# Optimization experiments

Measured on AMD Instinct MI355X. Metric: run time of the kernel, lower is better.

## Reference

```python
import jax, jax.numpy as jnp
import numpy as np

B, T, D, H = 4, 2048, 1024, 16
DH = D // H


def setup_inputs() -> dict:
    key = jax.random.key(0)
    ks = jax.random.split(key, 11)
    s = 1.0 / np.sqrt(D)
    return {
        "q": jax.random.normal(ks[0], (B, T, D), jnp.float32),
        "k": jax.random.normal(ks[1], (B, T, D), jnp.float32),
        "v": jax.random.normal(ks[2], (B, T, D), jnp.float32),
        "Wq": jax.random.normal(ks[3], (D, D), jnp.float32) * s,
        "bq": jax.random.normal(ks[4], (D,), jnp.float32) * s,
        "Wk": jax.random.normal(ks[5], (D, D), jnp.float32) * s,
        "bk": jax.random.normal(ks[6], (D,), jnp.float32) * s,
        "Wv": jax.random.normal(ks[7], (D, D), jnp.float32) * s,
        "bv": jax.random.normal(ks[8], (D,), jnp.float32) * s,
        "Wo": jax.random.normal(ks[9], (D, D), jnp.float32) * s,
        "bo": jax.random.normal(ks[10], (D,), jnp.float32) * s,
    }


def _heads(x):
    # (B, T, D) -> (B, H, T, DH)
    return x.reshape(B, T, H, DH).transpose(0, 2, 1, 3)


def reference(q, k, v, Wq, bq, Wk, bk, Wv, bv, Wo, bo):
    qh = _heads(q @ Wq + bq)
    kh = _heads(k @ Wk + bk)
    vh = _heads(v @ Wv + bv)
    scale = 1.0 / np.sqrt(DH).astype(np.float32)
    # full (B, H, T, T) score matrix, as in the original module
    scores = jnp.einsum("bhqd,bhkd->bhqk", qh, kh) * scale
    causal = jnp.tril(jnp.ones((T, T), dtype=bool))  # keep j <= i (causal intent)
    scores = jnp.where(causal, scores, -jnp.inf)
    attn = jax.nn.softmax(scores, axis=-1)
    ctx = jnp.einsum("bhqk,bhkd->bhqd", attn, vh)
    ctx = ctx.transpose(0, 2, 1, 3).reshape(B, T, D)
    return ctx @ Wo + bo
```

## Files before the change

### kernel.cpp

```cpp
#include <hip/hip_runtime.h>
#include <hip/hip_bf16.h>

#define NB 4
#define NT 2048
#define ND 1024
#define NH 16
#define NDH 64
#define NM (NB*NT)

typedef __bf16 bf16_t;
typedef bf16_t bf16x4 __attribute__((ext_vector_type(4)));
typedef bf16_t bf16x8 __attribute__((ext_vector_type(8)));
typedef float f32x2 __attribute__((ext_vector_type(2)));
typedef float f32x4 __attribute__((ext_vector_type(4)));
typedef unsigned int u32x4 __attribute__((ext_vector_type(4)));

__device__ __forceinline__ void gload_lds16(const bf16_t* g, bf16_t* l) {
  __builtin_amdgcn_global_load_lds(
      (const __attribute__((address_space(1))) unsigned int*)g,
      (__attribute__((address_space(3))) unsigned int*)l, 16, 0, 0);
}

__device__ __forceinline__ f32x2 lo2(f32x4 v) { return __builtin_shufflevector(v, v, 0, 1); }
__device__ __forceinline__ f32x2 hi2(f32x4 v) { return __builtin_shufflevector(v, v, 2, 3); }

__device__ __forceinline__ float exp2_hw(float x) {
  float r;
  asm("v_exp_f32 %0, %1" : "=v"(r) : "v"(x));
  return r;
}

__global__ void transpose_cvt4(const float* __restrict__ w0, const float* __restrict__ w1,
                               const float* __restrict__ w2, const float* __restrict__ w3,
                               bf16_t* __restrict__ o0, bf16_t* __restrict__ o1,
                               bf16_t* __restrict__ o2, bf16_t* __restrict__ o3) {
  __shared__ float tile[32][33];
  const float* in = blockIdx.z == 0 ? w0 : blockIdx.z == 1 ? w1 : blockIdx.z == 2 ? w2 : w3;
  bf16_t* out     = blockIdx.z == 0 ? o0 : blockIdx.z == 1 ? o1 : blockIdx.z == 2 ? o2 : o3;
  int n0 = blockIdx.x * 32, k0 = blockIdx.y * 32;
  int tx = threadIdx.x & 31, ty = threadIdx.x >> 5;
  #pragma unroll
  for (int r = ty; r < 32; r += 8)
    tile[r][tx] = in[(size_t)(k0 + r) * ND + n0 + tx];
  __syncthreads();
  #pragma unroll
  for (int r = ty; r < 32; r += 8)
    out[(size_t)(n0 + r) * ND + k0 + tx] = (bf16_t)tile[tx][r];
}

#define ALD 36
__global__ __launch_bounds__(256) void gemm_qkv(
    const float* __restrict__ Aq, const float* __restrict__ Ak, const float* __restrict__ Av,
    const bf16_t* __restrict__ Bq, const bf16_t* __restrict__ Bk, const bf16_t* __restrict__ Bv,
    const float* __restrict__ bq, const float* __restrict__ bk, const float* __restrict__ bv,
    bf16_t* __restrict__ Qh, bf16_t* __restrict__ Kh, bf16_t* __restrict__ Vt,
    float qscale) {
  __shared__ bf16_t As[128 * ALD];
  __shared__ bf16_t Bs[128 * 32];
  const int z = blockIdx.z;
  const float*  A    = z == 0 ? Aq : z == 1 ? Ak : Av;
  const bf16_t* Bt   = z == 0 ? Bq : z == 1 ? Bk : Bv;
  const float*  bias = z == 0 ? bq : z == 1 ? bk : bv;
  const float   scale = z == 0 ? qscale : 1.0f;
  bf16_t* outp = z == 0 ? Qh : z == 1 ? Kh : Vt;

  const int tid  = threadIdx.x;
  const int lane = tid & 63;
  const int wid  = tid >> 6;
  const int tm = blockIdx.x * 128;
  const int tn = blockIdx.y * 128;
  const int wr = wid >> 1, wc = wid & 1;
  const int lrow = lane & 15;
  const int lko  = (lane >> 4) << 3;

  const int cB  = wid * 64 + lane;
  const int rB0 = cB >> 2;
  const int kB0 = (cB & 3) << 3;

  const int arow = tid >> 1;
  const int acb  = (tid & 1) << 4;
  const float* abase = A + (size_t)(tm + arow) * ND + acb;

  f32x4 acc[4][4];
  #pragma unroll
  for (int i = 0; i < 4; ++i)
    #pragma unroll
    for (int j = 0; j < 4; ++j) {
      f32x4 z4 = {0.f, 0.f, 0.f, 0.f};
      acc[i][j] = z4;
    }

  float4 ar0 = ((const float4*)abase)[0];
  float4 ar1 = ((const float4*)abase)[1];
  float4 ar2 = ((const float4*)abase)[2];
  float4 ar3 = ((const float4*)abase)[3];

  for (int k0 = 0; k0 < ND; k0 += 32) {
    gload_lds16(Bt + (size_t)(tn + rB0)      * ND + k0 + kB0, Bs + wid * 512);
    gload_lds16(Bt + (size_t)(tn + rB0 + 64) * ND + k0 + kB0, Bs + 2048 + wid * 512);

    bf16x8 w0, w1;
    w0[0] = (bf16_t)ar0.x; w0[1] = (bf16_t)ar0.y; w0[2] = (bf16_t)ar0.z; w0[3] = (bf16_t)ar0.w;
    w0[4] = (bf16_t)ar1.x; w0[5] = (bf16_t)ar1.y; w0[6] = (bf16_t)ar1.z; w0[7] = (bf16_t)ar1.w;
    w1[0] = (bf16_t)ar2.x; w1[1] = (bf16_t)ar2.y; w1[2] = (bf16_t)ar2.z; w1[3] = (bf16_t)ar2.w;
    w1[4] = (bf16_t)ar3.x; w1[5] = (bf16_t)ar3.y; w1[6] = (bf16_t)ar3.z; w1[7] = (bf16_t)ar3.w;
    *(bf16x8*)&As[arow * ALD + acb]     = w0;
    *(bf16x8*)&As[arow * ALD + acb + 8] = w1;

    asm volatile("s_waitcnt vmcnt(0) lgkmcnt(0)\n\ts_barrier" ::: "memory");

    if (k0 + 32 < ND) {
      const float4* ap = (const float4*)(abase + k0 + 32);
      ar0 = ap[0]; ar1 = ap[1]; ar2 = ap[2]; ar3 = ap[3];
    }

    bf16x8 af[4], bfr[4];
    #pragma unroll
    for (int i = 0; i < 4; ++i)
      af[i] = *(const bf16x8*)&As[(wr * 64 + i * 16 + lrow) * ALD + lko];
    #pragma unroll
    for (int j = 0; j < 4; ++j)
      bfr[j] = *(const bf16x8*)&Bs[(wc * 64 + j * 16 + lrow) * 32 + lko];
    #pragma unroll
    for (int i = 0; i < 4; ++i)
      #pragma unroll
      for (int j = 0; j < 4; ++j)
        acc[i][j] = __builtin_amdgcn_mfma_f32_16x16x32_bf16(af[i], bfr[j], acc[i][j], 0, 0, 0);

    asm volatile("s_waitcnt lgkmcnt(0)\n\ts_barrier" ::: "memory");
  }

  const int rb = (lane >> 4) << 2;
  #pragma unroll
  for (int j = 0; j < 4; ++j) {
    int n = tn + wc * 64 + j * 16 + lrow;
    float bv = bias[n];
    int h = n >> 6, dh = n & (NDH - 1);
    #pragma unroll
    for (int i = 0; i < 4; ++i) {
      int m0 = tm + wr * 64 + i * 16 + rb;
      int b = m0 >> 11, t0 = m0 & (NT - 1);
      if (z == 2) {
        bf16x4 o;
        #pragma unroll
        for (int r = 0; r < 4; ++r) o[r] = (bf16_t)((acc[i][j][r] + bv) * scale);
        size_t idx = ((size_t)(b * NH + h) * NDH + dh) * NT + t0;
        *(bf16x4*)(outp + idx) = o;
      } else {
        #pragma unroll
        for (int r = 0; r < 4; ++r) {
          float val = (acc[i][j][r] + bv) * scale;
          size_t idx = ((size_t)(b * NH + h) * NT + t0 + r) * NDH + dh;
          outp[idx] = (bf16_t)val;
        }
      }
    }
  }
}

__global__ __launch_bounds__(256) void gemm_out(const bf16_t* __restrict__ A,
                                                const bf16_t* __restrict__ Bt,
                                                const float* __restrict__ bias,
                                                float* __restrict__ outp) {
  __shared__ bf16_t As[128 * 32];
  __shared__ bf16_t Bs[128 * 32];
  const int tid  = threadIdx.x;
  const int lane = tid & 63;
  const int wid  = tid >> 6;
  const int tm = blockIdx.x * 128;
  const int tn = blockIdx.y * 128;
  const int wr = wid >> 1, wc = wid & 1;
  const int lrow = lane & 15;
  const int lko  = (lane >> 4) << 3;

  const int cA  = wid * 64 + lane;
  const int rA0 = cA >> 2;
  const int kA0 = (cA & 3) << 3;

  f32x4 acc[4][4];
  #pragma unroll
  for (int i = 0; i < 4; ++i)
    #pragma unroll
    for (int j = 0; j < 4; ++j) {
      f32x4 z = {0.f, 0.f, 0.f, 0.f};
      acc[i][j] = z;
    }

  for (int k0 = 0; k0 < ND; k0 += 32) {
    gload_lds16(A  + (size_t)(tm + rA0)      * ND + k0 + kA0, As + wid * 512);
    gload_lds16(A  + (size_t)(tm + rA0 + 64) * ND + k0 + kA0, As + 2048 + wid * 512);
    gload_lds16(Bt + (size_t)(tn + rA0)      * ND + k0 + kA0, Bs + wid * 512);
    gload_lds16(Bt + (size_t)(tn + rA0 + 64) * ND + k0 + kA0, Bs + 2048 + wid * 512);
    __syncthreads();
    bf16x8 af[4], bfr[4];
    #pragma unroll
    for (int i = 0; i < 4; ++i)
      af[i] = *(const bf16x8*)&As[(wr * 64 + i * 16 + lrow) * 32 + lko];
    #pragma unroll
    for (int j = 0; j < 4; ++j)
      bfr[j] = *(const bf16x8*)&Bs[(wc * 64 + j * 16 + lrow) * 32 + lko];
    #pragma unroll
    for (int i = 0; i < 4; ++i)
      #pragma unroll
      for (int j = 0; j < 4; ++j)
        acc[i][j] = __builtin_amdgcn_mfma_f32_16x16x32_bf16(af[i], bfr[j], acc[i][j], 0, 0, 0);
    __syncthreads();
  }

  const int rb = (lane >> 4) << 2;
  #pragma unroll
  for (int j = 0; j < 4; ++j) {
    int n = tn + wc * 64 + j * 16 + lrow;
    float bv = bias[n];
    #pragma unroll
    for (int i = 0; i < 4; ++i) {
      #pragma unroll
      for (int r = 0; r < 4; ++r) {
        int m = tm + wr * 64 + i * 16 + rb + r;
        outp[(size_t)m * ND + n] = acc[i][j][r] + bv;
      }
    }
  }
}


__device__ __forceinline__ bf16x8 lds_swz_read(const bf16_t* base, int row, int colb) {
  return *(const bf16x8*)((const char*)base + row * 128 + (colb ^ ((row & 7) << 4)));
}

#define CVTPK(lo, hi) ({ unsigned r_; \
  asm("v_cvt_pk_bf16_f32 %0, %1, %2" : "=v"(r_) : "v"(lo), "v"(hi)); r_; })

__global__ __launch_bounds__(256) void attn_kernel(
    const bf16_t* __restrict__ Qh, const bf16_t* __restrict__ Kh,
    const bf16_t* __restrict__ Vt, bf16_t* __restrict__ ctx) {
  __shared__ bf16_t Ks[2][64 * 64];
  __shared__ bf16_t Vs[2][64 * 64];
  const int tid  = threadIdx.x;
  const int lane = tid & 63;
  const int wid  = tid >> 6;

  const int work    = (blockIdx.x & 7) * 128 + (blockIdx.x >> 3);
  const int bh      = work >> 4;
  const int pairIdx = work & 15;
  const int b = bh >> 4, h = bh & 15;

  const bf16_t* Qbh = Qh + (size_t)bh * NT * NDH;
  const bf16_t* Kbh = Kh + (size_t)bh * NT * NDH;
  const bf16_t* Vbh = Vt + (size_t)bh * NDH * NT;

  const int lrow = lane & 15;
  const int lg   = lane >> 4;

  const char *kS0, *kS1, *vS0, *vS1;
  {
    int o0 = wid * 1024 + lane * 16;
    int o1 = 4096 + wid * 1024 + lane * 16;
    int r0_ = o0 >> 7, r1_ = o1 >> 7;
    kS0 = (const char*)Kbh + (o0 ^ ((r0_ & 7) << 4));
    kS1 = (const char*)Kbh + (o1 ^ ((r1_ & 7) << 4));
    int c0 = (o0 & 127) ^ ((r0_ & 7) << 4);
    int c1 = (o1 & 127) ^ ((r1_ & 7) << 4);
    vS0 = (const char*)Vbh + (size_t)r0_ * (NT * 2) + c0;
    vS1 = (const char*)Vbh + (size_t)r1_ * (NT * 2) + c1;
  }
  const int ldsOff = wid * 512;

  auto stage = [&](int t, int buf) {
    bf16_t* kb = Ks[buf];
    bf16_t* vb = Vs[buf];
    size_t kOff = (size_t)t * 8192;
    size_t vOff = (size_t)t * 128;
    gload_lds16((const bf16_t*)(kS0 + kOff), kb + ldsOff);
    gload_lds16((const bf16_t*)(kS1 + kOff), kb + 2048 + ldsOff);
    gload_lds16((const bf16_t*)(vS0 + vOff), vb + ldsOff);
    gload_lds16((const bf16_t*)(vS1 + vOff), vb + 2048 + ldsOff);
  };

  #pragma unroll 1
  for (int half = 0; half < 2; ++half) {
    const int qidx = half ? (31 - pairIdx) : pairIdx;
    const int r0   = qidx * 64 + wid * 16;
    const int qg   = r0 + lrow;

    bf16x8 qf0 = *(const bf16x8*)&Qbh[(size_t)(r0 + lrow) * NDH + lg * 8];
    bf16x8 qf1 = *(const bf16x8*)&Qbh[(size_t)(r0 + lrow) * NDH + 32 + lg * 8];

    float lsum = 0.f;
    f32x4 acc[4];
    #pragma unroll
    for (int d = 0; d < 4; ++d) { f32x4 z = {0.f, 0.f, 0.f, 0.f}; acc[d] = z; }

    __syncthreads();
    stage(0, 0);
    int cur = 0;

    #pragma unroll 1
    for (int t = 0; t <= qidx; ++t) {
      asm volatile("s_waitcnt vmcnt(0)\n\ts_barrier" ::: "memory");
      if (t < qidx) stage(t + 1, cur ^ 1);

      const bf16_t* ksCur = Ks[cur];
      const bf16_t* vsCur = Vs[cur];

      f32x4 sg[4];
      #pragma unroll
      for (int g = 0; g < 4; ++g) { f32x4 z = {0.f, 0.f, 0.f, 0.f}; sg[g] = z; }
      __builtin_amdgcn_s_setprio(1);
      #pragma unroll
      for (int g = 0; g < 4; ++g) {
        bf16x8 kfa = lds_swz_read(ksCur, g * 16 + lrow, lg * 16);
        sg[g] = __builtin_amdgcn_mfma_f32_16x16x32_bf16(kfa, qf0, sg[g], 0, 0, 0);
        bf16x8 kfb = lds_swz_read(ksCur, g * 16 + lrow, 64 + lg * 16);
        sg[g] = __builtin_amdgcn_mfma_f32_16x16x32_bf16(kfb, qf1, sg[g], 0, 0, 0);
      }
      __builtin_amdgcn_s_setprio(0);

      if (t == qidx) {
        const int jb = t * 64;
        #pragma unroll
        for (int g = 0; g < 4; ++g)
          #pragma unroll
          for (int r = 0; r < 4; ++r)
            if (jb + g * 16 + lg * 4 + r > qg) sg[g][r] = -1e30f;
      }

      #pragma unroll
      for (int g = 0; g < 4; ++g)
        #pragma unroll
        for (int r = 0; r < 4; ++r) sg[g][r] = exp2_hw(sg[g][r]);
      f32x2 s2 = (lo2(sg[0]) + hi2(sg[0])) + (lo2(sg[1]) + hi2(sg[1]));
      s2 += (lo2(sg[2]) + hi2(sg[2])) + (lo2(sg[3]) + hi2(sg[3]));
      lsum += s2[0] + s2[1];

      unsigned W00 = CVTPK(sg[0][0], sg[0][1]), W01 = CVTPK(sg[0][2], sg[0][3]);
      unsigned W10 = CVTPK(sg[1][0], sg[1][1]), W11 = CVTPK(sg[1][2], sg[1][3]);
      unsigned W20 = CVTPK(sg[2][0], sg[2][1]), W21 = CVTPK(sg[2][2], sg[2][3]);
      unsigned W30 = CVTPK(sg[3][0], sg[3][1]), W31 = CVTPK(sg[3][2], sg[3][3]);
      unsigned w00, w01, w02, w03, w10, w11, w12, w13;
      { unsigned a = W00, bb = W10;
        asm("v_permlane32_swap_b32 %0, %1" : "+v"(a), "+v"(bb));
        asm("v_permlane16_swap_b32 %0, %1" : "+v"(a), "+v"(bb));
        w00 = a; w02 = bb; }
      { unsigned a = W01, bb = W11;
        asm("v_permlane32_swap_b32 %0, %1" : "+v"(a), "+v"(bb));
        asm("v_permlane16_swap_b32 %0, %1" : "+v"(a), "+v"(bb));
        w01 = a; w03 = bb; }
      { unsigned a = W20, bb = W30;
        asm("v_permlane32_swap_b32 %0, %1" : "+v"(a), "+v"(bb));
        asm("v_permlane16_swap_b32 %0, %1" : "+v"(a), "+v"(bb));
        w10 = a; w12 = bb; }
      { unsigned a = W21, bb = W31;
        asm("v_permlane32_swap_b32 %0, %1" : "+v"(a), "+v"(bb));
        asm("v_permlane16_swap_b32 %0, %1" : "+v"(a), "+v"(bb));
        w11 = a; w13 = bb; }
      u32x4 c0 = {w00, w01, w02, w03};
      u32x4 c1 = {w10, w11, w12, w13};
      bf16x8 pf0 = __builtin_bit_cast(bf16x8, c0);
      bf16x8 pf1 = __builtin_bit_cast(bf16x8, c1);

      __builtin_amdgcn_s_setprio(1);
      #pragma unroll
      for (int d = 0; d < 4; ++d) {
        bf16x8 vf0 = lds_swz_read(vsCur, d * 16 + lrow, lg * 16);
        acc[d] = __builtin_amdgcn_mfma_f32_16x16x32_bf16(vf0, pf0, acc[d], 0, 0, 0);
        bf16x8 vf1 = lds_swz_read(vsCur, d * 16 + lrow, 64 + lg * 16);
        acc[d] = __builtin_amdgcn_mfma_f32_16x16x32_bf16(vf1, pf1, acc[d], 0, 0, 0);
      }
      __builtin_amdgcn_s_setprio(0);

      cur ^= 1;
    }

    float ps = lsum;
    ps += __shfl_xor(ps, 16);
    ps += __shfl_xor(ps, 32);
    float inv = 1.f / ps;
    f32x4 inv4 = {inv, inv, inv, inv};
    size_t orow = ((size_t)b * NT + qg) * ND + h * NDH;
    #pragma unroll
    for (int d2 = 0; d2 < 4; ++d2) {
      f32x4 vv = acc[d2] * inv4;
      bf16x4 o;
      #pragma unroll
      for (int r = 0; r < 4; ++r) o[r] = (bf16_t)vv[r];
      *(bf16x4*)&ctx[orow + d2 * 16 + lg * 4] = o;
    }
  }
}

extern "C" void kernel_launch(void* const* d_in, const int* in_sizes, int n_in,
                              void* d_out, int out_size, void* d_ws, size_t ws_size,
                              hipStream_t stream) {
  const float* q  = (const float*)d_in[0];
  const float* k  = (const float*)d_in[1];
  const float* v  = (const float*)d_in[2];
  const float* Wq = (const float*)d_in[3];
  const float* bq = (const float*)d_in[4];
  const float* Wk = (const float*)d_in[5];
  const float* bk = (const float*)d_in[6];
  const float* Wv = (const float*)d_in[7];
  const float* bv = (const float*)d_in[8];
  const float* Wo = (const float*)d_in[9];
  const float* bo = (const float*)d_in[10];
  float* out = (float*)d_out;

  char* ws = (char*)d_ws;
  const size_t szMK = (size_t)NM * ND * sizeof(bf16_t);
  const size_t szW  = (size_t)ND * ND * sizeof(bf16_t);
  bf16_t* ctx = (bf16_t*)(ws);
  bf16_t* Qh  = (bf16_t*)(ws + szMK);
  bf16_t* Kh  = (bf16_t*)(ws + 2 * szMK);
  bf16_t* Vt  = (bf16_t*)(ws + 3 * szMK);
  bf16_t* Wqt = (bf16_t*)(ws + 4 * szMK);
  bf16_t* Wkt = (bf16_t*)(ws + 4 * szMK + szW);
  bf16_t* Wvt = (bf16_t*)(ws + 4 * szMK + 2 * szW);
  bf16_t* Wot = (bf16_t*)(ws + 4 * szMK + 3 * szW);

  dim3 tb(256);
  transpose_cvt4<<<dim3(ND / 32, ND / 32, 4), tb, 0, stream>>>(Wq, Wk, Wv, Wo,
                                                               Wqt, Wkt, Wvt, Wot);

  const float qscale = 0.125f * 1.44269504f;

  gemm_qkv<<<dim3(NM / 128, ND / 128, 3), tb, 0, stream>>>(
      q, k, v, Wqt, Wkt, Wvt, bq, bk, bv, Qh, Kh, Vt, qscale);

  attn_kernel<<<dim3(NB * NH * 16), tb, 0, stream>>>(Qh, Kh, Vt, ctx);

  gemm_out<<<dim3(NM / 128, ND / 128), tb, 0, stream>>>(ctx, Wot, bo, out);
}
```

Baseline: 202.5 us.

## Process two 16-row query groups per wave in attention, halving block size

New measurement: 204.8 us. No clear change (+1.1%).

```diff
diff --git a/kernel.cpp b/kernel.cpp
--- a/kernel.cpp
+++ b/kernel.cpp
@@ -231,7 +231,35 @@
 #define CVTPK(lo, hi) ({ unsigned r_; \
   asm("v_cvt_pk_bf16_f32 %0, %1, %2" : "=v"(r_) : "v"(lo), "v"(hi)); r_; })
 
-__global__ __launch_bounds__(256) void attn_kernel(
+#define PTRANS(sg, pf0, pf1) do { \
+    unsigned W00 = CVTPK(sg[0][0], sg[0][1]), W01 = CVTPK(sg[0][2], sg[0][3]); \
+    unsigned W10 = CVTPK(sg[1][0], sg[1][1]), W11 = CVTPK(sg[1][2], sg[1][3]); \
+    unsigned W20 = CVTPK(sg[2][0], sg[2][1]), W21 = CVTPK(sg[2][2], sg[2][3]); \
+    unsigned W30 = CVTPK(sg[3][0], sg[3][1]), W31 = CVTPK(sg[3][2], sg[3][3]); \
+    unsigned w00, w01, w02, w03, w10, w11, w12, w13; \
+    { unsigned a = W00, bb = W10; \
+      asm("v_permlane32_swap_b32 %0, %1" : "+v"(a), "+v"(bb)); \
+      asm("v_permlane16_swap_b32 %0, %1" : "+v"(a), "+v"(bb)); \
+      w00 = a; w02 = bb; } \
+    { unsigned a = W01, bb = W11; \
+      asm("v_permlane32_swap_b32 %0, %1" : "+v"(a), "+v"(bb)); \
+      asm("v_permlane16_swap_b32 %0, %1" : "+v"(a), "+v"(bb)); \
+      w01 = a; w03 = bb; } \
+    { unsigned a = W20, bb = W30; \
+      asm("v_permlane32_swap_b32 %0, %1" : "+v"(a), "+v"(bb)); \
+      asm("v_permlane16_swap_b32 %0, %1" : "+v"(a), "+v"(bb)); \
+      w10 = a; w12 = bb; } \
+    { unsigned a = W21, bb = W31; \
+      asm("v_permlane32_swap_b32 %0, %1" : "+v"(a), "+v"(bb)); \
+      asm("v_permlane16_swap_b32 %0, %1" : "+v"(a), "+v"(bb)); \
+      w11 = a; w13 = bb; } \
+    u32x4 c0 = {w00, w01, w02, w03}; \
+    u32x4 c1 = {w10, w11, w12, w13}; \
+    pf0 = __builtin_bit_cast(bf16x8, c0); \
+    pf1 = __builtin_bit_cast(bf16x8, c1); \
+  } while (0)
+
+__global__ __launch_bounds__(128) void attn_kernel(
     const bf16_t* __restrict__ Qh, const bf16_t* __restrict__ Kh,
     const bf16_t* __restrict__ Vt, bf16_t* __restrict__ ctx) {
   __shared__ bf16_t Ks[2][64 * 64];
@@ -252,44 +280,58 @@
   const int lrow = lane & 15;
   const int lg   = lane >> 4;
 
-  const char *kS0, *kS1, *vS0, *vS1;
+  const char *kS0, *kS1, *kS2, *kS3, *vS0, *vS1, *vS2, *vS3;
   {
-    int o0 = wid * 1024 + lane * 16;
-    int o1 = 4096 + wid * 1024 + lane * 16;
-    int r0_ = o0 >> 7, r1_ = o1 >> 7;
-    kS0 = (const char*)Kbh + (o0 ^ ((r0_ & 7) << 4));
-    kS1 = (const char*)Kbh + (o1 ^ ((r1_ & 7) << 4));
-    int c0 = (o0 & 127) ^ ((r0_ & 7) << 4);
-    int c1 = (o1 & 127) ^ ((r1_ & 7) << 4);
-    vS0 = (const char*)Vbh + (size_t)r0_ * (NT * 2) + c0;
-    vS1 = (const char*)Vbh + (size_t)r1_ * (NT * 2) + c1;
-  }
-  const int ldsOff = wid * 512;
+    int o, row;
+    o = 0 * 2048 + wid * 1024 + lane * 16; row = o >> 7;
+    kS0 = (const char*)Kbh + (o ^ ((row & 7) << 4));
+    vS0 = (const char*)Vbh + (size_t)row * (NT * 2) + ((o & 127) ^ ((row & 7) << 4));
+    o = 1 * 2048 + wid * 1024 + lane * 16; row = o >> 7;
+    kS1 = (const char*)Kbh + (o ^ ((row & 7) << 4));
+    vS1 = (const char*)Vbh + (size_t)row * (NT * 2) + ((o & 127) ^ ((row & 7) << 4));
+    o = 2 * 2048 + wid * 1024 + lane * 16; row = o >> 7;
+    kS2 = (const char*)Kbh + (o ^ ((row & 7) << 4));
+    vS2 = (const char*)Vbh + (size_t)row * (NT * 2) + ((o & 127) ^ ((row & 7) << 4));
+    o = 3 * 2048 + wid * 1024 + lane * 16; row = o >> 7;
+    kS3 = (const char*)Kbh + (o ^ ((row & 7) << 4));
+    vS3 = (const char*)Vbh + (size_t)row * (NT * 2) + ((o & 127) ^ ((row & 7) << 4));
+  }
+  const int w512 = wid * 512;
 
   auto stage = [&](int t, int buf) {
     bf16_t* kb = Ks[buf];
     bf16_t* vb = Vs[buf];
     size_t kOff = (size_t)t * 8192;
     size_t vOff = (size_t)t * 128;
-    gload_lds16((const bf16_t*)(kS0 + kOff), kb + ldsOff);
-    gload_lds16((const bf16_t*)(kS1 + kOff), kb + 2048 + ldsOff);
-    gload_lds16((const bf16_t*)(vS0 + vOff), vb + ldsOff);
-    gload_lds16((const bf16_t*)(vS1 + vOff), vb + 2048 + ldsOff);
+    gload_lds16((const bf16_t*)(kS0 + kOff), kb + w512);
+    gload_lds16((const bf16_t*)(kS1 + kOff), kb + 1024 + w512);
+    gload_lds16((const bf16_t*)(kS2 + kOff), kb + 2048 + w512);
+    gload_lds16((const bf16_t*)(kS3 + kOff), kb + 3072 + w512);
+    gload_lds16((const bf16_t*)(vS0 + vOff), vb + w512);
+    gload_lds16((const bf16_t*)(vS1 + vOff), vb + 1024 + w512);
+    gload_lds16((const bf16_t*)(vS2 + vOff), vb + 2048 + w512);
+    gload_lds16((const bf16_t*)(vS3 + vOff), vb + 3072 + w512);
   };
 
   #pragma unroll 1
   for (int half = 0; half < 2; ++half) {
     const int qidx = half ? (31 - pairIdx) : pairIdx;
-    const int r0   = qidx * 64 + wid * 16;
-    const int qg   = r0 + lrow;
-
-    bf16x8 qf0 = *(const bf16x8*)&Qbh[(size_t)(r0 + lrow) * NDH + lg * 8];
-    bf16x8 qf1 = *(const bf16x8*)&Qbh[(size_t)(r0 + lrow) * NDH + 32 + lg * 8];
-
-    float lsum = 0.f;
-    f32x4 acc[4];
-    #pragma unroll
-    for (int d = 0; d < 4; ++d) { f32x4 z = {0.f, 0.f, 0.f, 0.f}; acc[d] = z; }
+    const int r0   = qidx * 64;
+    const int qa   = r0 + wid * 32 + lrow;
+    const int qb   = qa + 16;
+
+    bf16x8 qf0a = *(const bf16x8*)&Qbh[(size_t)qa * NDH + lg * 8];
+    bf16x8 qf1a = *(const bf16x8*)&Qbh[(size_t)qa * NDH + 32 + lg * 8];
+    bf16x8 qf0b = *(const bf16x8*)&Qbh[(size_t)qb * NDH + lg * 8];
+    bf16x8 qf1b = *(const bf16x8*)&Qbh[(size_t)qb * NDH + 32 + lg * 8];
+
+    float lsa = 0.f, lsb = 0.f;
+    f32x4 acca[4], accb[4];
+    #pragma unroll
+    for (int d = 0; d < 4; ++d) {
+      f32x4 z = {0.f, 0.f, 0.f, 0.f};
+      acca[d] = z; accb[d] = z;
+    }
 
     __syncthreads();
     stage(0, 0);
@@ -303,16 +345,21 @@
       const bf16_t* ksCur = Ks[cur];
       const bf16_t* vsCur = Vs[cur];
 
-      f32x4 sg[4];
-      #pragma unroll
-      for (int g = 0; g < 4; ++g) { f32x4 z = {0.f, 0.f, 0.f, 0.f}; sg[g] = z; }
+      f32x4 sa[4], sb[4];
+      #pragma unroll
+      for (int g = 0; g < 4; ++g) {
+        f32x4 z = {0.f, 0.f, 0.f, 0.f};
+        sa[g] = z; sb[g] = z;
+      }
       __builtin_amdgcn_s_setprio(1);
       #pragma unroll
       for (int g = 0; g < 4; ++g) {
         bf16x8 kfa = lds_swz_read(ksCur, g * 16 + lrow, lg * 16);
-        sg[g] = __builtin_amdgcn_mfma_f32_16x16x32_bf16(kfa, qf0, sg[g], 0, 0, 0);
+        sa[g] = __builtin_amdgcn_mfma_f32_16x16x32_bf16(kfa, qf0a, sa[g], 0, 0, 0);
+        sb[g] = __builtin_amdgcn_mfma_f32_16x16x32_bf16(kfa, qf0b, sb[g], 0, 0, 0);
         bf16x8 kfb = lds_swz_read(ksCur, g * 16 + lrow, 64 + lg * 16);
-        sg[g] = __builtin_amdgcn_mfma_f32_16x16x32_bf16(kfb, qf1, sg[g], 0, 0, 0);
+        sa[g] = __builtin_amdgcn_mfma_f32_16x16x32_bf16(kfb, qf1a, sa[g], 0, 0, 0);
+        sb[g] = __builtin_amdgcn_mfma_f32_16x16x32_bf16(kfb, qf1b, sb[g], 0, 0, 0);
       }
       __builtin_amdgcn_s_setprio(0);
 
@@ -321,70 +368,79 @@
         #pragma unroll
         for (int g = 0; g < 4; ++g)
           #pragma unroll
-          for (int r = 0; r < 4; ++r)
-            if (jb + g * 16 + lg * 4 + r > qg) sg[g][r] = -1e30f;
+          for (int r = 0; r < 4; ++r) {
+            int kv = jb + g * 16 + lg * 4 + r;
+            if (kv > qa) sa[g][r] = -1e30f;
+            if (kv > qb) sb[g][r] = -1e30f;
+          }
       }
 
       #pragma unroll
       for (int g = 0; g < 4; ++g)
         #pragma unroll
-        for (int r = 0; r < 4; ++r) sg[g][r] = exp2_hw(sg[g][r]);
-      f32x2 s2 = (lo2(sg[0]) + hi2(sg[0])) + (lo2(sg[1]) + hi2(sg[1]));
-      s2 += (lo2(sg[2]) + hi2(sg[2])) + (lo2(sg[3]) + hi2(sg[3]));
-      lsum += s2[0] + s2[1];
-
-      unsigned W00 = CVTPK(sg[0][0], sg[0][1]), W01 = CVTPK(sg[0][2], sg[0][3]);
-      unsigned W10 = CVTPK(sg[1][0], sg[1][1]), W11 = CVTPK(sg[1][2], sg[1][3]);
-      unsigned W20 = CVTPK(sg[2][0], sg[2][1]), W21 = CVTPK(sg[2][2], sg[2][3]);
-      unsigned W30 = CVTPK(sg[3][0], sg[3][1]), W31 = CVTPK(sg[3][2], sg[3][3]);
-      unsigned w00, w01, w02, w03, w10, w11, w12, w13;
-      { unsigned a = W00, bb = W10;
-        asm("v_permlane32_swap_b32 %0, %1" : "+v"(a), "+v"(bb));
-        asm("v_permlane16_swap_b32 %0, %1" : "+v"(a), "+v"(bb));
-        w00 = a; w02 = bb; }
-      { unsigned a = W01, bb = W11;
-        asm("v_permlane32_swap_b32 %0, %1" : "+v"(a), "+v"(bb));
-        asm("v_permlane16_swap_b32 %0, %1" : "+v"(a), "+v"(bb));
-        w01 = a; w03 = bb; }
-      { unsigned a = W20, bb = W30;
-        asm("v_permlane32_swap_b32 %0, %1" : "+v"(a), "+v"(bb));
-        asm("v_permlane16_swap_b32 %0, %1" : "+v"(a), "+v"(bb));
-        w10 = a; w12 = bb; }
-      { unsigned a = W21, bb = W31;
-        asm("v_permlane32_swap_b32 %0, %1" : "+v"(a), "+v"(bb));
-        asm("v_permlane16_swap_b32 %0, %1" : "+v"(a), "+v"(bb));
-        w11 = a; w13 = bb; }
-      u32x4 c0 = {w00, w01, w02, w03};
-      u32x4 c1 = {w10, w11, w12, w13};
-      bf16x8 pf0 = __builtin_bit_cast(bf16x8, c0);
-      bf16x8 pf1 = __builtin_bit_cast(bf16x8, c1);
+        for (int r = 0; r < 4; ++r) {
+          sa[g][r] = exp2_hw(sa[g][r]);
+          sb[g][r] = exp2_hw(sb[g][r]);
+        }
+      {
+        f32x2 s2 = (lo2(sa[0]) + hi2(sa[0])) + (lo2(sa[1]) + hi2(sa[1]));
+        s2 += (lo2(sa[2]) + hi2(sa[2])) + (lo2(sa[3]) + hi2(sa[3]));
+        lsa += s2[0] + s2[1];
+        f32x2 t2 = (lo2(sb[0]) + hi2(sb[0])) + (lo2(sb[1]) + hi2(sb[1]));
+        t2 += (lo2(sb[2]) + hi2(sb[2])) + (lo2(sb[3]) + hi2(sb[3]));
+        lsb += t2[0] + t2[1];
+      }
+
+      bf16x8 pf0a, pf1a, pf0b, pf1b;
+      PTRANS(sa, pf0a, pf1a);
+      PTRANS(sb, pf0b, pf1b);
 
       __builtin_amdgcn_s_setprio(1);
       #pragma unroll
       for (int d = 0; d < 4; ++d) {
         bf16x8 vf0 = lds_swz_read(vsCur, d * 16 + lrow, lg * 16);
-        acc[d] = __builtin_amdgcn_mfma_f32_16x16x32_bf16(vf0, pf0, acc[d], 0, 0, 0);
+        acca[d] = __builtin_amdgcn_mfma_f32_16x16x32_bf16(vf0, pf0a, acca[d], 0, 0, 0);
+        accb[d] = __builtin_amdgcn_mfma_f32_16x16x32_bf16(vf0, pf0b, accb[d], 0, 0, 0);
         bf16x8 vf1 = lds_swz_read(vsCur, d * 16 + lrow, 64 + lg * 16);
-        acc[d] = __builtin_amdgcn_mfma_f32_16x16x32_bf16(vf1, pf1, acc[d], 0, 0, 0);
+        acca[d] = __builtin_amdgcn_mfma_f32_16x16x32_bf16(vf1, pf1a, acca[d], 0, 0, 0);
+        accb[d] = __builtin_amdgcn_mfma_f32_16x16x32_bf16(vf1, pf1b, accb[d], 0, 0, 0);
       }
       __builtin_amdgcn_s_setprio(0);
 
       cur ^= 1;
     }
 
-    float ps = lsum;
-    ps += __shfl_xor(ps, 16);
-    ps += __shfl_xor(ps, 32);
-    float inv = 1.f / ps;
-    f32x4 inv4 = {inv, inv, inv, inv};
-    size_t orow = ((size_t)b * NT + qg) * ND + h * NDH;
-    #pragma unroll
-    for (int d2 = 0; d2 < 4; ++d2) {
-      f32x4 vv = acc[d2] * inv4;
-      bf16x4 o;
-      #pragma unroll
-      for (int r = 0; r < 4; ++r) o[r] = (bf16_t)vv[r];
-      *(bf16x4*)&ctx[orow + d2 * 16 + lg * 4] = o;
+    {
+      float ps = lsa;
+      ps += __shfl_xor(ps, 16);
+      ps += __shfl_xor(ps, 32);
+      float inv = 1.f / ps;
+      f32x4 inv4 = {inv, inv, inv, inv};
+      size_t orow = ((size_t)b * NT + qa) * ND + h * NDH;
+      #pragma unroll
+      for (int d2 = 0; d2 < 4; ++d2) {
+        f32x4 vv = acca[d2] * inv4;
+        bf16x4 o;
+        #pragma unroll
+        for (int r = 0; r < 4; ++r) o[r] = (bf16_t)vv[r];
+        *(bf16x4*)&ctx[orow + d2 * 16 + lg * 4] = o;
+      }
+    }
+    {
+      float ps = lsb;
+      ps += __shfl_xor(ps, 16);
+      ps += __shfl_xor(ps, 32);
+      float inv = 1.f / ps;
+      f32x4 inv4 = {inv, inv, inv, inv};
+      size_t orow = ((size_t)b * NT + qb) * ND + h * NDH;
+      #pragma unroll
+      for (int d2 = 0; d2 < 4; ++d2) {
+        f32x4 vv = accb[d2] * inv4;
+        bf16x4 o;
+        #pragma unroll
+        for (int r = 0; r < 4; ++r) o[r] = (bf16_t)vv[r];
+        *(bf16x4*)&ctx[orow + d2 * 16 + lg * 4] = o;
+      }
     }
   }
 }
@@ -426,7 +482,7 @@
   gemm_qkv<<<dim3(NM / 128, ND / 128, 3), tb, 0, stream>>>(
       q, k, v, Wqt, Wkt, Wvt, bq, bk, bv, Qh, Kh, Vt, qscale);
 
-  attn_kernel<<<dim3(NB * NH * 16), tb, 0, stream>>>(Qh, Kh, Vt, ctx);
+  attn_kernel<<<dim3(NB * NH * 16), dim3(128), 0, stream>>>(Qh, Kh, Vt, ctx);
 
   gemm_out<<<dim3(NM / 128, ND / 128), tb, 0, stream>>>(ctx, Wot, bo, out);
 }
```

## Double-buffer LDS tiles in QKV and output projection GEMMs

Applied to the files above, without the earlier changes.

New measurement: 212.8 us. +5.1%, slower.

```diff
diff --git a/kernel.cpp b/kernel.cpp
--- a/kernel.cpp
+++ b/kernel.cpp
@@ -55,8 +55,8 @@
     const float* __restrict__ bq, const float* __restrict__ bk, const float* __restrict__ bv,
     bf16_t* __restrict__ Qh, bf16_t* __restrict__ Kh, bf16_t* __restrict__ Vt,
     float qscale) {
-  __shared__ bf16_t As[128 * ALD];
-  __shared__ bf16_t Bs[128 * 32];
+  __shared__ bf16_t As[2][128 * ALD];
+  __shared__ bf16_t Bs[2][128 * 32];
   const int z = blockIdx.z;
   const float*  A    = z == 0 ? Aq : z == 1 ? Ak : Av;
   const bf16_t* Bt   = z == 0 ? Bq : z == 1 ? Bk : Bv;
@@ -76,6 +76,8 @@
   const int cB  = wid * 64 + lane;
   const int rB0 = cB >> 2;
   const int kB0 = (cB & 3) << 3;
+  const bf16_t* bbase0 = Bt + (size_t)(tn + rB0) * ND + kB0;
+  const bf16_t* bbase1 = Bt + (size_t)(tn + rB0 + 64) * ND + kB0;
 
   const int arow = tid >> 1;
   const int acb  = (tid & 1) << 4;
@@ -90,44 +92,70 @@
       acc[i][j] = z4;
     }
 
-  float4 ar0 = ((const float4*)abase)[0];
-  float4 ar1 = ((const float4*)abase)[1];
-  float4 ar2 = ((const float4*)abase)[2];
-  float4 ar3 = ((const float4*)abase)[3];
-
-  for (int k0 = 0; k0 < ND; k0 += 32) {
-    gload_lds16(Bt + (size_t)(tn + rB0)      * ND + k0 + kB0, Bs + wid * 512);
-    gload_lds16(Bt + (size_t)(tn + rB0 + 64) * ND + k0 + kB0, Bs + 2048 + wid * 512);
-
+  float4 ar0, ar1, ar2, ar3;
+
+  {
+    const float4* ap = (const float4*)abase;
+    ar0 = ap[0]; ar1 = ap[1]; ar2 = ap[2]; ar3 = ap[3];
+  }
+  {
     bf16x8 w0, w1;
     w0[0] = (bf16_t)ar0.x; w0[1] = (bf16_t)ar0.y; w0[2] = (bf16_t)ar0.z; w0[3] = (bf16_t)ar0.w;
     w0[4] = (bf16_t)ar1.x; w0[5] = (bf16_t)ar1.y; w0[6] = (bf16_t)ar1.z; w0[7] = (bf16_t)ar1.w;
     w1[0] = (bf16_t)ar2.x; w1[1] = (bf16_t)ar2.y; w1[2] = (bf16_t)ar2.z; w1[3] = (bf16_t)ar2.w;
     w1[4] = (bf16_t)ar3.x; w1[5] = (bf16_t)ar3.y; w1[6] = (bf16_t)ar3.z; w1[7] = (bf16_t)ar3.w;
-    *(bf16x8*)&As[arow * ALD + acb]     = w0;
-    *(bf16x8*)&As[arow * ALD + acb + 8] = w1;
-
-    asm volatile("s_waitcnt vmcnt(0) lgkmcnt(0)\n\ts_barrier" ::: "memory");
-
-    if (k0 + 32 < ND) {
-      const float4* ap = (const float4*)(abase + k0 + 32);
+    *(bf16x8*)&As[0][arow * ALD + acb]     = w0;
+    *(bf16x8*)&As[0][arow * ALD + acb + 8] = w1;
+  }
+  gload_lds16(bbase0, &Bs[0][wid * 512]);
+  gload_lds16(bbase1, &Bs[0][2048 + wid * 512]);
+  {
+    const float4* ap = (const float4*)(abase + 32);
+    ar0 = ap[0]; ar1 = ap[1]; ar2 = ap[2]; ar3 = ap[3];
+  }
+  asm volatile("s_waitcnt vmcnt(4) lgkmcnt(0)\n\ts_barrier" ::: "memory");
+
+  int cur = 0;
+  for (int k0 = 0; k0 < ND; k0 += 32) {
+    const bool hasNext  = (k0 + 32 < ND);
+    const bool hasNext2 = (k0 + 64 < ND);
+
+    if (hasNext) {
+      bf16x8 w0, w1;
+      w0[0] = (bf16_t)ar0.x; w0[1] = (bf16_t)ar0.y; w0[2] = (bf16_t)ar0.z; w0[3] = (bf16_t)ar0.w;
+      w0[4] = (bf16_t)ar1.x; w0[5] = (bf16_t)ar1.y; w0[6] = (bf16_t)ar1.z; w0[7] = (bf16_t)ar1.w;
+      w1[0] = (bf16_t)ar2.x; w1[1] = (bf16_t)ar2.y; w1[2] = (bf16_t)ar2.z; w1[3] = (bf16_t)ar2.w;
+      w1[4] = (bf16_t)ar3.x; w1[5] = (bf16_t)ar3.y; w1[6] = (bf16_t)ar3.z; w1[7] = (bf16_t)ar3.w;
+      *(bf16x8*)&As[cur ^ 1][arow * ALD + acb]     = w0;
+      *(bf16x8*)&As[cur ^ 1][arow * ALD + acb + 8] = w1;
+      gload_lds16(bbase0 + k0 + 32, &Bs[cur ^ 1][wid * 512]);
+      gload_lds16(bbase1 + k0 + 32, &Bs[cur ^ 1][2048 + wid * 512]);
+    }
+    if (hasNext2) {
+      const float4* ap = (const float4*)(abase + k0 + 64);
       ar0 = ap[0]; ar1 = ap[1]; ar2 = ap[2]; ar3 = ap[3];
     }
 
     bf16x8 af[4], bfr[4];
     #pragma unroll
     for (int i = 0; i < 4; ++i)
-      af[i] = *(const bf16x8*)&As[(wr * 64 + i * 16 + lrow) * ALD + lko];
+      af[i] = *(const bf16x8*)&As[cur][(wr * 64 + i * 16 + lrow) * ALD + lko];
     #pragma unroll
     for (int j = 0; j < 4; ++j)
-      bfr[j] = *(const bf16x8*)&Bs[(wc * 64 + j * 16 + lrow) * 32 + lko];
+      bfr[j] = *(const bf16x8*)&Bs[cur][(wc * 64 + j * 16 + lrow) * 32 + lko];
     #pragma unroll
     for (int i = 0; i < 4; ++i)
       #pragma unroll
       for (int j = 0; j < 4; ++j)
         acc[i][j] = __builtin_amdgcn_mfma_f32_16x16x32_bf16(af[i], bfr[j], acc[i][j], 0, 0, 0);
 
-    asm volatile("s_waitcnt lgkmcnt(0)\n\ts_barrier" ::: "memory");
+    if (hasNext) {
+      if (hasNext2)
+        asm volatile("s_waitcnt vmcnt(4) lgkmcnt(0)\n\ts_barrier" ::: "memory");
+      else
+        asm volatile("s_waitcnt vmcnt(0) lgkmcnt(0)\n\ts_barrier" ::: "memory");
+      cur ^= 1;
+    }
   }
 
   const int rb = (lane >> 4) << 2;
@@ -162,8 +190,8 @@
                                                 const bf16_t* __restrict__ Bt,
                                                 const float* __restrict__ bias,
                                                 float* __restrict__ outp) {
-  __shared__ bf16_t As[128 * 32];
-  __shared__ bf16_t Bs[128 * 32];
+  __shared__ bf16_t As[2][128 * 32];
+  __shared__ bf16_t Bs[2][128 * 32];
   const int tid  = threadIdx.x;
   const int lane = tid & 63;
   const int wid  = tid >> 6;
@@ -176,6 +204,10 @@
   const int cA  = wid * 64 + lane;
   const int rA0 = cA >> 2;
   const int kA0 = (cA & 3) << 3;
+  const bf16_t* a0 = A  + (size_t)(tm + rA0)      * ND + kA0;
+  const bf16_t* a1 = A  + (size_t)(tm + rA0 + 64) * ND + kA0;
+  const bf16_t* b0 = Bt + (size_t)(tn + rA0)      * ND + kA0;
+  const bf16_t* b1 = Bt + (size_t)(tn + rA0 + 64) * ND + kA0;
 
   f32x4 acc[4][4];
   #pragma unroll
@@ -186,25 +218,38 @@
       acc[i][j] = z;
     }
 
+  auto stage = [&](int k0, int buf) {
+    gload_lds16(a0 + k0, &As[buf][wid * 512]);
+    gload_lds16(a1 + k0, &As[buf][2048 + wid * 512]);
+    gload_lds16(b0 + k0, &Bs[buf][wid * 512]);
+    gload_lds16(b1 + k0, &Bs[buf][2048 + wid * 512]);
+  };
+
+  stage(0, 0);
+  asm volatile("s_waitcnt vmcnt(0)\n\ts_barrier" ::: "memory");
+
+  int cur = 0;
   for (int k0 = 0; k0 < ND; k0 += 32) {
-    gload_lds16(A  + (size_t)(tm + rA0)      * ND + k0 + kA0, As + wid * 512);
-    gload_lds16(A  + (size_t)(tm + rA0 + 64) * ND + k0 + kA0, As + 2048 + wid * 512);
-    gload_lds16(Bt + (size_t)(tn + rA0)      * ND + k0 + kA0, Bs + wid * 512);
-    gload_lds16(Bt + (size_t)(tn + rA0 + 64) * ND + k0 + kA0, Bs + 2048 + wid * 512);
-    __syncthreads();
+    const bool hasNext = (k0 + 32 < ND);
+    if (hasNext) stage(k0 + 32, cur ^ 1);
+
     bf16x8 af[4], bfr[4];
     #pragma unroll
     for (int i = 0; i < 4; ++i)
-      af[i] = *(const bf16x8*)&As[(wr * 64 + i * 16 + lrow) * 32 + lko];
+      af[i] = *(const bf16x8*)&As[cur][(wr * 64 + i * 16 + lrow) * 32 + lko];
     #pragma unroll
     for (int j = 0; j < 4; ++j)
-      bfr[j] = *(const bf16x8*)&Bs[(wc * 64 + j * 16 + lrow) * 32 + lko];
+      bfr[j] = *(const bf16x8*)&Bs[cur][(wc * 64 + j * 16 + lrow) * 32 + lko];
     #pragma unroll
     for (int i = 0; i < 4; ++i)
       #pragma unroll
       for (int j = 0; j < 4; ++j)
         acc[i][j] = __builtin_amdgcn_mfma_f32_16x16x32_bf16(af[i], bfr[j], acc[i][j], 0, 0, 0);
-    __syncthreads();
+
+    if (hasNext) {
+      asm volatile("s_waitcnt vmcnt(0) lgkmcnt(0)\n\ts_barrier" ::: "memory");
+      cur ^= 1;
+    }
   }
 
   const int rb = (lane >> 4) << 2;
```

## Pre-convert QKV inputs to bf16 and use 256x256 pipelined 8-wave projection GEMM

Applied to the files above, without the earlier changes.

Measured after the change: 196.9 us. -2.7%, faster.

```diff
diff --git a/kernel.cpp b/kernel.cpp
--- a/kernel.cpp
+++ b/kernel.cpp
@@ -48,109 +48,156 @@
     out[(size_t)(n0 + r) * ND + k0 + tx] = (bf16_t)tile[tx][r];
 }
 
-#define ALD 36
-__global__ __launch_bounds__(256) void gemm_qkv(
-    const float* __restrict__ Aq, const float* __restrict__ Ak, const float* __restrict__ Av,
+__global__ void cvt3(const float* __restrict__ q, const float* __restrict__ k,
+                     const float* __restrict__ v, bf16_t* __restrict__ oq,
+                     bf16_t* __restrict__ ok, bf16_t* __restrict__ ov) {
+  const float* in = blockIdx.y == 0 ? q : blockIdx.y == 1 ? k : v;
+  bf16_t* out     = blockIdx.y == 0 ? oq : blockIdx.y == 1 ? ok : ov;
+  int i = blockIdx.x * 256 + threadIdx.x;
+  float4 vv = ((const float4*)in)[i];
+  bf16x4 o;
+  o[0] = (bf16_t)vv.x; o[1] = (bf16_t)vv.y; o[2] = (bf16_t)vv.z; o[3] = (bf16_t)vv.w;
+  ((bf16x4*)out)[i] = o;
+}
+
+__global__ __launch_bounds__(512, 2) void gemm8_qkv(
+    const bf16_t* __restrict__ Aq, const bf16_t* __restrict__ Ak, const bf16_t* __restrict__ Av,
     const bf16_t* __restrict__ Bq, const bf16_t* __restrict__ Bk, const bf16_t* __restrict__ Bv,
     const float* __restrict__ bq, const float* __restrict__ bk, const float* __restrict__ bv,
     bf16_t* __restrict__ Qh, bf16_t* __restrict__ Kh, bf16_t* __restrict__ Vt,
     float qscale) {
-  __shared__ bf16_t As[128 * ALD];
-  __shared__ bf16_t Bs[128 * 32];
+  __shared__ bf16_t S[2][4][8192];
   const int z = blockIdx.z;
-  const float*  A    = z == 0 ? Aq : z == 1 ? Ak : Av;
+  const bf16_t* A    = z == 0 ? Aq : z == 1 ? Ak : Av;
   const bf16_t* Bt   = z == 0 ? Bq : z == 1 ? Bk : Bv;
   const float*  bias = z == 0 ? bq : z == 1 ? bk : bv;
   const float   scale = z == 0 ? qscale : 1.0f;
   bf16_t* outp = z == 0 ? Qh : z == 1 ? Kh : Vt;
 
-  const int tid  = threadIdx.x;
-  const int lane = tid & 63;
-  const int wid  = tid >> 6;
-  const int tm = blockIdx.x * 128;
-  const int tn = blockIdx.y * 128;
-  const int wr = wid >> 1, wc = wid & 1;
-  const int lrow = lane & 15;
-  const int lko  = (lane >> 4) << 3;
-
-  const int cB  = wid * 64 + lane;
-  const int rB0 = cB >> 2;
-  const int kB0 = (cB & 3) << 3;
-
-  const int arow = tid >> 1;
-  const int acb  = (tid & 1) << 4;
-  const float* abase = A + (size_t)(tm + arow) * ND + acb;
-
-  f32x4 acc[4][4];
-  #pragma unroll
-  for (int i = 0; i < 4; ++i)
-    #pragma unroll
-    for (int j = 0; j < 4; ++j) {
-      f32x4 z4 = {0.f, 0.f, 0.f, 0.f};
-      acc[i][j] = z4;
-    }
-
-  float4 ar0 = ((const float4*)abase)[0];
-  float4 ar1 = ((const float4*)abase)[1];
-  float4 ar2 = ((const float4*)abase)[2];
-  float4 ar3 = ((const float4*)abase)[3];
-
-  for (int k0 = 0; k0 < ND; k0 += 32) {
-    gload_lds16(Bt + (size_t)(tn + rB0)      * ND + k0 + kB0, Bs + wid * 512);
-    gload_lds16(Bt + (size_t)(tn + rB0 + 64) * ND + k0 + kB0, Bs + 2048 + wid * 512);
-
-    bf16x8 w0, w1;
-    w0[0] = (bf16_t)ar0.x; w0[1] = (bf16_t)ar0.y; w0[2] = (bf16_t)ar0.z; w0[3] = (bf16_t)ar0.w;
-    w0[4] = (bf16_t)ar1.x; w0[5] = (bf16_t)ar1.y; w0[6] = (bf16_t)ar1.z; w0[7] = (bf16_t)ar1.w;
-    w1[0] = (bf16_t)ar2.x; w1[1] = (bf16_t)ar2.y; w1[2] = (bf16_t)ar2.z; w1[3] = (bf16_t)ar2.w;
-    w1[4] = (bf16_t)ar3.x; w1[5] = (bf16_t)ar3.y; w1[6] = (bf16_t)ar3.z; w1[7] = (bf16_t)ar3.w;
-    *(bf16x8*)&As[arow * ALD + acb]     = w0;
-    *(bf16x8*)&As[arow * ALD + acb + 8] = w1;
-
-    asm volatile("s_waitcnt vmcnt(0) lgkmcnt(0)\n\ts_barrier" ::: "memory");
-
-    if (k0 + 32 < ND) {
-      const float4* ap = (const float4*)(abase + k0 + 32);
-      ar0 = ap[0]; ar1 = ap[1]; ar2 = ap[2]; ar3 = ap[3];
-    }
-
-    bf16x8 af[4], bfr[4];
-    #pragma unroll
-    for (int i = 0; i < 4; ++i)
-      af[i] = *(const bf16x8*)&As[(wr * 64 + i * 16 + lrow) * ALD + lko];
-    #pragma unroll
-    for (int j = 0; j < 4; ++j)
-      bfr[j] = *(const bf16x8*)&Bs[(wc * 64 + j * 16 + lrow) * 32 + lko];
-    #pragma unroll
-    for (int i = 0; i < 4; ++i)
-      #pragma unroll
-      for (int j = 0; j < 4; ++j)
-        acc[i][j] = __builtin_amdgcn_mfma_f32_16x16x32_bf16(af[i], bfr[j], acc[i][j], 0, 0, 0);
-
-    asm volatile("s_waitcnt lgkmcnt(0)\n\ts_barrier" ::: "memory");
-  }
-
-  const int rb = (lane >> 4) << 2;
-  #pragma unroll
-  for (int j = 0; j < 4; ++j) {
-    int n = tn + wc * 64 + j * 16 + lrow;
-    float bv = bias[n];
-    int h = n >> 6, dh = n & (NDH - 1);
-    #pragma unroll
-    for (int i = 0; i < 4; ++i) {
-      int m0 = tm + wr * 64 + i * 16 + rb;
-      int b = m0 >> 11, t0 = m0 & (NT - 1);
+  const int K = ND;
+  const int tid = threadIdx.x, lane = tid & 63, wid = tid >> 6;
+  const int wm = wid >> 2, wn = wid & 3;
+  const int lrow = lane & 15, lg = lane >> 4, rb = lg << 2;
+  const int tm = blockIdx.y * 256, tn = blockIdx.x * 256;
+
+  const int d0 = tid * 16, d1 = 8192 + tid * 16;
+  const int r0s = d0 >> 7, r1s = d1 >> 7;
+  const int cb0 = (d0 & 127) ^ ((r0s & 7) << 4);
+  const int cb1 = (d1 & 127) ^ ((r1s & 7) << 4);
+  const int e0 = d0 >> 1, e1 = d1 >> 1;
+  const bf16_t* aA0c0 = A  + (size_t)(tm + r0s) * K + (cb0 >> 1);
+  const bf16_t* aA0c1 = A  + (size_t)(tm + r1s) * K + (cb1 >> 1);
+  const bf16_t* aA1c0 = aA0c0 + (size_t)128 * K;
+  const bf16_t* aA1c1 = aA0c1 + (size_t)128 * K;
+  const bf16_t* bB0c0 = Bt + (size_t)(tn + r0s) * K + (cb0 >> 1);
+  const bf16_t* bB0c1 = Bt + (size_t)(tn + r1s) * K + (cb1 >> 1);
+  const bf16_t* bB1c0 = bB0c0 + (size_t)128 * K;
+  const bf16_t* bB1c1 = bB0c1 + (size_t)128 * K;
+
+  const int swz = (lrow & 7) << 4;
+  const int kc0 = (lg * 16) ^ swz;
+  const int kc1 = (64 + lg * 16) ^ swz;
+  const int aOffBase = lrow * 128;
+  const int bOffBase = (wn & 1) * 8192 + lrow * 128;
+
+  f32x4 acc[8][4];
+  #pragma unroll
+  for (int m = 0; m < 8; ++m)
+    #pragma unroll
+    for (int n = 0; n < 4; ++n) {
+      f32x4 zz = {0.f, 0.f, 0.f, 0.f};
+      acc[m][n] = zz;
+    }
+
+  gload_lds16(bB0c0, &S[0][2][0] + e0); gload_lds16(bB0c1, &S[0][2][0] + e1);
+  gload_lds16(bB1c0, &S[0][3][0] + e0); gload_lds16(bB1c1, &S[0][3][0] + e1);
+  gload_lds16(aA0c0, &S[0][0][0] + e0); gload_lds16(aA0c1, &S[0][0][0] + e1);
+  gload_lds16(aA1c0, &S[0][1][0] + e0); gload_lds16(aA1c1, &S[0][1][0] + e1);
+  gload_lds16(bB0c0 + 64, &S[1][2][0] + e0); gload_lds16(bB0c1 + 64, &S[1][2][0] + e1);
+  gload_lds16(bB1c0 + 64, &S[1][3][0] + e0); gload_lds16(bB1c1 + 64, &S[1][3][0] + e1);
+  asm volatile("s_waitcnt vmcnt(4)\n\ts_barrier" ::: "memory");
+
+  const int NS = K / 64;
+  #pragma unroll 1
+  for (int s = 0; s < NS; ++s) {
+    const int b = s & 1;
+    const char* aReg = (const char*)&S[b][wm][0];
+    const char* bReg = (const char*)&S[b][2 + (wn >> 1)][0];
+    bf16x8 bfr[4][2];
+
+    #pragma unroll
+    for (int p = 0; p < 4; ++p) {
+      if (p == 0) {
+        #pragma unroll
+        for (int n = 0; n < 4; ++n) {
+          bfr[n][0] = *(const bf16x8*)(bReg + n * 2048 + bOffBase + kc0);
+          bfr[n][1] = *(const bf16x8*)(bReg + n * 2048 + bOffBase + kc1);
+        }
+      }
+      bf16x8 afr[2][2];
+      afr[0][0] = *(const bf16x8*)(aReg + (2 * p)     * 2048 + aOffBase + kc0);
+      afr[0][1] = *(const bf16x8*)(aReg + (2 * p)     * 2048 + aOffBase + kc1);
+      afr[1][0] = *(const bf16x8*)(aReg + (2 * p + 1) * 2048 + aOffBase + kc0);
+      afr[1][1] = *(const bf16x8*)(aReg + (2 * p + 1) * 2048 + aOffBase + kc1);
+
+      if (p == 0 && s + 1 < NS) {
+        gload_lds16(aA0c0 + (s + 1) * 64, &S[b ^ 1][0][0] + e0);
+        gload_lds16(aA0c1 + (s + 1) * 64, &S[b ^ 1][0][0] + e1);
+      }
+      if (p == 1 && s + 1 < NS) {
+        gload_lds16(aA1c0 + (s + 1) * 64, &S[b ^ 1][1][0] + e0);
+        gload_lds16(aA1c1 + (s + 1) * 64, &S[b ^ 1][1][0] + e1);
+      }
+      if (p == 2 && s + 2 < NS) {
+        gload_lds16(bB0c0 + (s + 2) * 64, &S[b][2][0] + e0);
+        gload_lds16(bB0c1 + (s + 2) * 64, &S[b][2][0] + e1);
+      }
+      if (p == 3 && s + 2 < NS) {
+        gload_lds16(bB1c0 + (s + 2) * 64, &S[b][3][0] + e0);
+        gload_lds16(bB1c1 + (s + 2) * 64, &S[b][3][0] + e1);
+      }
+
+      asm volatile("s_barrier" ::: "memory");
+      __builtin_amdgcn_s_setprio(1);
+      #pragma unroll
+      for (int mm = 0; mm < 2; ++mm)
+        #pragma unroll
+        for (int n = 0; n < 4; ++n)
+          #pragma unroll
+          for (int kk = 0; kk < 2; ++kk)
+            acc[2 * p + mm][n] = __builtin_amdgcn_mfma_f32_16x16x32_bf16(
+                afr[mm][kk], bfr[n][kk], acc[2 * p + mm][n], 0, 0, 0);
+      __builtin_amdgcn_s_setprio(0);
+      if (p < 3)
+        asm volatile("s_waitcnt lgkmcnt(0)\n\ts_barrier" ::: "memory");
+    }
+
+    if (s < NS - 2)
+      asm volatile("s_waitcnt vmcnt(4) lgkmcnt(0)\n\ts_barrier" ::: "memory");
+    else if (s == NS - 2)
+      asm volatile("s_waitcnt vmcnt(0) lgkmcnt(0)\n\ts_barrier" ::: "memory");
+  }
+
+  #pragma unroll
+  for (int n = 0; n < 4; ++n) {
+    const int ncol = tn + wn * 64 + n * 16 + lrow;
+    const float bv = bias[ncol];
+    const int h = ncol >> 6, dh = ncol & (NDH - 1);
+    #pragma unroll
+    for (int m = 0; m < 8; ++m) {
+      const int m0 = tm + wm * 128 + m * 16 + rb;
+      const int bb = m0 >> 11, t0 = m0 & (NT - 1);
       if (z == 2) {
         bf16x4 o;
         #pragma unroll
-        for (int r = 0; r < 4; ++r) o[r] = (bf16_t)((acc[i][j][r] + bv) * scale);
-        size_t idx = ((size_t)(b * NH + h) * NDH + dh) * NT + t0;
+        for (int r = 0; r < 4; ++r) o[r] = (bf16_t)(acc[m][n][r] + bv);
+        size_t idx = ((size_t)(bb * NH + h) * NDH + dh) * NT + t0;
         *(bf16x4*)(outp + idx) = o;
       } else {
         #pragma unroll
         for (int r = 0; r < 4; ++r) {
-          float val = (acc[i][j][r] + bv) * scale;
-          size_t idx = ((size_t)(b * NH + h) * NT + t0 + r) * NDH + dh;
+          float val = (acc[m][n][r] + bv) * scale;
+          size_t idx = ((size_t)(bb * NH + h) * NT + t0 + r) * NDH + dh;
           outp[idx] = (bf16_t)val;
         }
       }
@@ -222,7 +269,6 @@
     }
   }
 }
-
 
 __device__ __forceinline__ bf16x8 lds_swz_read(const bf16_t* base, int row, int colb) {
   return *(const bf16x8*)((const char*)base + row * 128 + (colb ^ ((row & 7) << 4)));
@@ -408,6 +454,9 @@
   char* ws = (char*)d_ws;
   const size_t szMK = (size_t)NM * ND * sizeof(bf16_t);
   const size_t szW  = (size_t)ND * ND * sizeof(bf16_t);
+  bf16_t* Xq  = (bf16_t*)d_out;
+  bf16_t* Xk  = Xq + (size_t)NM * ND;
+  bf16_t* Xv  = (bf16_t*)(ws);
   bf16_t* ctx = (bf16_t*)(ws);
   bf16_t* Qh  = (bf16_t*)(ws + szMK);
   bf16_t* Kh  = (bf16_t*)(ws + 2 * szMK);
@@ -423,8 +472,10 @@
 
   const float qscale = 0.125f * 1.44269504f;
 
-  gemm_qkv<<<dim3(NM / 128, ND / 128, 3), tb, 0, stream>>>(
-      q, k, v, Wqt, Wkt, Wvt, bq, bk, bv, Qh, Kh, Vt, qscale);
+  cvt3<<<dim3(NM * ND / 4 / 256, 3), tb, 0, stream>>>(q, k, v, Xq, Xk, Xv);
+
+  gemm8_qkv<<<dim3(ND / 256, NM / 256, 3), dim3(512), 0, stream>>>(
+      Xq, Xk, Xv, Wqt, Wkt, Wvt, bq, bk, bv, Qh, Kh, Vt, qscale);
 
   attn_kernel<<<dim3(NB * NH * 16), tb, 0, stream>>>(Qh, Kh, Vt, ctx);
 
```
